# Performance work log

Measured on AMD Instinct MI355X. Metric: run time of the kernel, lower is better.

The kernel has to match this reference:

```python
import jax, jax.numpy as jnp
import numpy as np

# ---- static config (mirrors MonitorRetina init) ----
N, S, H, W = 256, 1, 144, 256        # stimulus: [N, S, H, W]
HR, WR = 144, 256                    # retina height/width
FOV_HALF_RAD = 0.5 * 75.0 * np.pi / 180.0   # Angular retina, degrees=75
GELU_GAMMA = 1.7015043497085571      # variance-preserving gain for gelu
OUT_OF_RANGE = 10.0                  # grid value for rays missing the monitor


def isotropic_grid_2d(h, w):
    """Pixel-center coordinates, isotropic (normalized by max dim), [-1,1] on the long axis."""
    m = float(max(h, w))
    y = (jnp.arange(h, dtype=jnp.float32) * 2.0 + 1.0 - h) / m
    x = (jnp.arange(w, dtype=jnp.float32) * 2.0 + 1.0 - w) / m
    gy, gx = jnp.meshgrid(y, x, indexing="ij")
    return gx, gy  # each [h, w]


def rmat_3d(ax, ay, az):
    """Batched 3D rotation matrix R = Rz @ Ry @ Rx from Euler angles, each [N]."""
    cx, sx = jnp.cos(ax), jnp.sin(ax)
    cy, sy = jnp.cos(ay), jnp.sin(ay)
    cz, sz = jnp.cos(az), jnp.sin(az)
    one, zero = jnp.ones_like(ax), jnp.zeros_like(ax)
    Rx = jnp.stack([one, zero, zero, zero, cx, -sx, zero, sx, cx], -1).reshape(-1, 3, 3)
    Ry = jnp.stack([cy, zero, sy, zero, one, zero, -sy, zero, cy], -1).reshape(-1, 3, 3)
    Rz = jnp.stack([cz, -sz, zero, sz, cz, zero, zero, zero, one], -1).reshape(-1, 3, 3)
    return jnp.einsum("nij,njk,nkl->nil", Rz, Ry, Rx)  # [N,3,3]


def retina_rays(rmat):
    """Angular retina: pixel angles -> unit ray directions, rotated per batch. [N,HR,WR,3]."""
    gx, gy = isotropic_grid_2d(HR, WR)
    ax, ay = gx * FOV_HALF_RAD, gy * FOV_HALF_RAD
    a = jnp.sqrt(ax * ax + ay * ay) + 1e-12
    sinc = jnp.sin(a) / a
    d = jnp.stack([sinc * ax, sinc * ay, jnp.cos(a)], -1)  # [HR,WR,3]
    return jnp.einsum("nij,hwj->nhwi", rmat, d)


def monitor_project(rays):
    """Plane monitor at unit distance along +z: perspective divide to isotropic grid coords. [N,HR,WR,2]."""
    rz = rays[..., 2]
    safe = rz > 1e-3
    inv = jnp.where(safe, rz, 1.0)
    gx = jnp.where(safe, rays[..., 0] / inv, OUT_OF_RANGE)
    gy = jnp.where(safe, rays[..., 1] / inv, OUT_OF_RANGE)
    return jnp.stack([gx, gy], -1)


def isotropic_grid_sample_2d(x, grid, pad_value=0.0):
    """Bilinear sample x:[N,C,H,W] at grid:[N,H',W',2] (isotropic coords), constant padding."""
    m = float(max(H, W))
    px = (grid[..., 0] * m + W - 1.0) * 0.5  # [N,H',W'] pixel coords
    py = (grid[..., 1] * m + H - 1.0) * 0.5
    x0 = jnp.floor(px)
    y0 = jnp.floor(py)
    wx = px - x0
    wy = py - y0
    x0i = x0.astype(jnp.int32)
    y0i = y0.astype(jnp.int32)

    def corner(img, yi, xi):
        valid = (xi >= 0) & (xi < W) & (yi >= 0) & (yi < H)
        v = img[:, jnp.clip(yi, 0, H - 1), jnp.clip(xi, 0, W - 1)]  # [C,H',W']
        return jnp.where(valid[None], v, pad_value)

    def one(img, y0i, x0i, wx, wy):
        v00 = corner(img, y0i, x0i)
        v01 = corner(img, y0i, x0i + 1)
        v10 = corner(img, y0i + 1, x0i)
        v11 = corner(img, y0i + 1, x0i + 1)
        return (v00 * (1 - wx) + v01 * wx) * (1 - wy) + (v10 * (1 - wx) + v11 * wx) * wy

    return jax.vmap(one)(x, y0i, x0i, wx, wy)  # [N,C,H',W']


def setup_inputs() -> dict:
    key = jax.random.key(0)
    ks = jax.random.split(key, 8)
    F, D = 16, 128
    return {
        "stimulus": jax.random.normal(ks[0], (N, S, H, W), jnp.float32),
        "perspective": jax.random.normal(ks[1], (N, F), jnp.float32),
        "W1": jax.random.normal(ks[2], (F, D), jnp.float32) / np.sqrt(F),
        "b1": jnp.zeros((D,), jnp.float32),
        "W2": jax.random.normal(ks[3], (D, D), jnp.float32) / np.sqrt(D),
        "b2": jnp.zeros((D,), jnp.float32),
        "Wp": jax.random.normal(ks[4], (D, 3), jnp.float32) * 0.05,  # proj gains init near 0
        "bp": jnp.zeros((3,), jnp.float32),
    }


def reference(stimulus, perspective, W1, b1, W2, b2, Wp, bp):
    # MLP -> 3 angles -> rotation matrix (rmat)
    h = jax.nn.gelu(perspective @ W1 + b1) * GELU_GAMMA
    h = jax.nn.gelu(h @ W2 + b2) * GELU_GAMMA
    ang = h @ Wp + bp                      # [N,3]
    rm = rmat_3d(ang[:, 0], ang[:, 1], ang[:, 2])
    rays = retina_rays(rm)                 # [N,HR,WR,3]
    grid = monitor_project(rays)           # [N,HR,WR,2]
    # monitor_pixel / retina_pixel are Raw (identity) transforms
    return isotropic_grid_sample_2d(stimulus, grid, pad_value=0.0)  # [N,S,HR,WR]
```

## Files before the change

### kernel.cpp

```cpp
#include <hip/hip_runtime.h>
#include <math.h>

#define NB    256
#define IMG_H 144
#define IMG_W 256
#define IMG_ELEMS (IMG_H * IMG_W)
#define LDS_STRIDE 260
#define HR    144
#define WR    256
#define FDIM  16
#define DDIM  128

#define FOV_HALF_RAD 0.6544984694978736f
#define GELU_GAMMA   1.7015043497085571f
#define OUT_OF_RANGE 10.0f

typedef float f32x4 __attribute__((ext_vector_type(4)));

__device__ __forceinline__ float gelu_gamma(float x) {
    const float k0 = 0.7978845608028654f;
    const float k1 = 0.044715f;
    float t = tanhf(k0 * (x + k1 * x * x * x));
    return 0.5f * x * (1.0f + t) * GELU_GAMMA;
}

__global__ void __launch_bounds__(DDIM) mlp_rmat_kernel(
    const float* __restrict__ persp,
    const float* __restrict__ W1,
    const float* __restrict__ b1,
    const float* __restrict__ W2,
    const float* __restrict__ b2,
    const float* __restrict__ Wp,
    const float* __restrict__ bp,
    float* __restrict__ Rout)
{
    const int n = blockIdx.x;
    const int d = threadIdx.x;

    __shared__ float sh1[DDIM];
    __shared__ float sh2[DDIM];
    __shared__ float ang[3];

    float acc = b1[d];
#pragma unroll
    for (int f = 0; f < FDIM; ++f)
        acc += persp[n * FDIM + f] * W1[f * DDIM + d];
    sh1[d] = gelu_gamma(acc);
    __syncthreads();

    float acc2 = b2[d];
#pragma unroll 8
    for (int k = 0; k < DDIM; ++k)
        acc2 += sh1[k] * W2[k * DDIM + d];
    sh2[d] = gelu_gamma(acc2);
    __syncthreads();

    if (d < 3) {
        float a = bp[d];
#pragma unroll 8
        for (int k = 0; k < DDIM; ++k)
            a += sh2[k] * Wp[k * 3 + d];
        ang[d] = a;
    }
    __syncthreads();

    if (d == 0) {
        float cx = cosf(ang[0]), sx = sinf(ang[0]);
        float cy = cosf(ang[1]), sy = sinf(ang[1]);
        float cz = cosf(ang[2]), sz = sinf(ang[2]);
        float* R = Rout + n * 9;
        R[0] = cz * cy;  R[1] = cz * sy * sx - sz * cx;  R[2] = cz * sy * cx + sz * sx;
        R[3] = sz * cy;  R[4] = sz * sy * sx + cz * cx;  R[5] = sz * sy * cx - cz * sx;
        R[6] = -sy;      R[7] = cy * sx;                 R[8] = cy * cx;
    }
}

__global__ void __launch_bounds__(1024, 4) retina_sample_kernel(
    const float* __restrict__ stim,
    const float* __restrict__ Rmat,
    float* __restrict__ out)
{
    __shared__ float simg[IMG_H * LDS_STRIDE];

    const int tid = threadIdx.x;
    const int n   = blockIdx.x;

    const float* Rn = Rmat + n * 9;
    const float r0 = Rn[0], r1 = Rn[1], r2 = Rn[2];
    const float r3 = Rn[3], r4 = Rn[4], r5 = Rn[5];
    const float r6 = Rn[6], r7 = Rn[7], r8 = Rn[8];

    const float* __restrict__ img = stim + (size_t)n * IMG_ELEMS;

    {
        const f32x4* __restrict__ src = (const f32x4*)img;
#pragma unroll
        for (int p = 0; p < 9; ++p) {
            const int g   = tid + p * 1024;
            const int row = g >> 6;
            const int c4  = g & 63;
            *(f32x4*)&simg[row * LDS_STRIDE + c4 * 4] = src[g];
        }
    }
    __syncthreads();

#pragma unroll
    for (int p = 0; p < 9; ++p) {
        const int g   = tid + p * 1024;
        const int px0 = g * 4;
        const int h   = px0 >> 8;
        const int w0  = px0 & 255;

        const float gy  = (2.0f * h + 1.0f - 144.0f) * (1.0f / 256.0f);
        const float ayv = gy * FOV_HALF_RAD;
        const float ay2 = ayv * ayv;

        float wx_[4], wy_[4];
        int a00[4], a01[4], a10[4], a11[4];
        bool m00[4], m01[4], m10[4], m11[4];

#pragma unroll
        for (int j = 0; j < 4; ++j) {
            const float gx  = (2.0f * (w0 + j) + 1.0f - 256.0f) * (1.0f / 256.0f);
            const float axv = gx * FOV_HALF_RAD;
            const float t   = axv * axv + ay2;

            float sc = fmaf(t, 2.7557319e-6f, -1.9841270e-4f);
            sc = fmaf(t, sc,  8.3333333e-3f);
            sc = fmaf(t, sc, -1.6666667e-1f);
            sc = fmaf(t, sc,  1.0f);

            float ca = fmaf(t, 2.4801587e-5f, -1.3888889e-3f);
            ca = fmaf(t, ca,  4.1666667e-2f);
            ca = fmaf(t, ca, -0.5f);
            ca = fmaf(t, ca,  1.0f);

            const float dx = sc * axv, dy = sc * ayv, dz = ca;

            const float rx = r0 * dx + r1 * dy + r2 * dz;
            const float ry = r3 * dx + r4 * dy + r5 * dz;
            const float rz = r6 * dx + r7 * dy + r8 * dz;

            const float inv = __builtin_amdgcn_rcpf(rz);
            const bool safe = rz > 0.001f;
            const float gxp = safe ? rx * inv : OUT_OF_RANGE;
            const float gyp = safe ? ry * inv : OUT_OF_RANGE;

            const float px = fmaf(gxp, 256.0f, (float)(IMG_W - 1)) * 0.5f;
            const float py = fmaf(gyp, 256.0f, (float)(IMG_H - 1)) * 0.5f;

            const float x0f = floorf(px), y0f = floorf(py);
            wx_[j] = px - x0f;
            wy_[j] = py - y0f;
            const int x0 = (int)x0f, y0 = (int)y0f;
            const int x1 = x0 + 1,   y1 = y0 + 1;

            const int xc0 = min(max(x0, 0), IMG_W - 1);
            const int xc1 = min(max(x1, 0), IMG_W - 1);
            const int yc0 = min(max(y0, 0), IMG_H - 1);
            const int yc1 = min(max(y1, 0), IMG_H - 1);

            m00[j] = ((unsigned)x0 < IMG_W) & ((unsigned)y0 < IMG_H);
            m01[j] = ((unsigned)x1 < IMG_W) & ((unsigned)y0 < IMG_H);
            m10[j] = ((unsigned)x0 < IMG_W) & ((unsigned)y1 < IMG_H);
            m11[j] = ((unsigned)x1 < IMG_W) & ((unsigned)y1 < IMG_H);

            a00[j] = yc0 * LDS_STRIDE + xc0;
            a01[j] = yc0 * LDS_STRIDE + xc1;
            a10[j] = yc1 * LDS_STRIDE + xc0;
            a11[j] = yc1 * LDS_STRIDE + xc1;
        }

        float v00[4], v01[4], v10[4], v11[4];
#pragma unroll
        for (int j = 0; j < 4; ++j) {
            v00[j] = simg[a00[j]];
            v01[j] = simg[a01[j]];
            v10[j] = simg[a10[j]];
            v11[j] = simg[a11[j]];
        }

        f32x4 res;
#pragma unroll
        for (int j = 0; j < 4; ++j) {
            const float c00 = m00[j] ? v00[j] : 0.0f;
            const float c01 = m01[j] ? v01[j] : 0.0f;
            const float c10 = m10[j] ? v10[j] : 0.0f;
            const float c11 = m11[j] ? v11[j] : 0.0f;
            const float top = c00 * (1.0f - wx_[j]) + c01 * wx_[j];
            const float bot = c10 * (1.0f - wx_[j]) + c11 * wx_[j];
            res[j] = top * (1.0f - wy_[j]) + bot * wy_[j];
        }

        f32x4* dst = (f32x4*)(out + (size_t)n * IMG_ELEMS + px0);
        __builtin_nontemporal_store(res, dst);
    }
}

extern "C" void kernel_launch(void* const* d_in, const int* in_sizes, int n_in,
                              void* d_out, int out_size, void* d_ws, size_t ws_size,
                              hipStream_t stream) {
    const float* stimulus    = (const float*)d_in[0];
    const float* perspective = (const float*)d_in[1];
    const float* W1          = (const float*)d_in[2];
    const float* b1          = (const float*)d_in[3];
    const float* W2          = (const float*)d_in[4];
    const float* b2          = (const float*)d_in[5];
    const float* Wp          = (const float*)d_in[6];
    const float* bp          = (const float*)d_in[7];
    float* out = (float*)d_out;

    float* Rmat = (float*)d_ws;

    mlp_rmat_kernel<<<NB, DDIM, 0, stream>>>(
        perspective, W1, b1, W2, b2, Wp, bp, Rmat);

    retina_sample_kernel<<<NB, 1024, 0, stream>>>(stimulus, Rmat, out);
}
```

Before: 118.7 us.

## Store stimulus in LDS as fp16 with zero border and split image across two blocks

```diff
diff --git a/kernel.cpp b/kernel.cpp
--- a/kernel.cpp
+++ b/kernel.cpp
@@ -5,17 +5,19 @@
 #define IMG_H 144
 #define IMG_W 256
 #define IMG_ELEMS (IMG_H * IMG_W)
-#define LDS_STRIDE 260
-#define HR    144
-#define WR    256
 #define FDIM  16
 #define DDIM  128
+
+#define LDS_STRIDE_H 264
+#define LDS_ROWS     (IMG_H + 2)
+#define SIDE_CELLS   (IMG_H * 8)
 
 #define FOV_HALF_RAD 0.6544984694978736f
 #define GELU_GAMMA   1.7015043497085571f
 #define OUT_OF_RANGE 10.0f
 
-typedef float f32x4 __attribute__((ext_vector_type(4)));
+typedef float    f32x4 __attribute__((ext_vector_type(4)));
+typedef _Float16 f16x4 __attribute__((ext_vector_type(4)));
 
 __device__ __forceinline__ float gelu_gamma(float x) {
     const float k0 = 0.7978845608028654f;
@@ -75,15 +77,16 @@
     }
 }
 
-__global__ void __launch_bounds__(1024, 4) retina_sample_kernel(
+__global__ void __launch_bounds__(1024, 8) retina_sample_kernel(
     const float* __restrict__ stim,
     const float* __restrict__ Rmat,
     float* __restrict__ out)
 {
-    __shared__ float simg[IMG_H * LDS_STRIDE];
-
-    const int tid = threadIdx.x;
-    const int n   = blockIdx.x;
+    __shared__ _Float16 simg[LDS_ROWS * LDS_STRIDE_H];
+
+    const int tid  = threadIdx.x;
+    const int n    = blockIdx.x;
+    const int half = blockIdx.y;
 
     const float* Rn = Rmat + n * 9;
     const float r0 = Rn[0], r1 = Rn[1], r2 = Rn[2];
@@ -92,6 +95,17 @@
 
     const float* __restrict__ img = stim + (size_t)n * IMG_ELEMS;
 
+    if (tid < LDS_STRIDE_H) {
+        simg[tid] = (_Float16)0.0f;
+        simg[(LDS_ROWS - 1) * LDS_STRIDE_H + tid] = (_Float16)0.0f;
+    }
+    for (int sb = tid; sb < SIDE_CELLS; sb += 1024) {
+        const int r = (sb >> 3) + 1;
+        int c = sb & 7;
+        c = (c < 4) ? c : (c + 256);
+        simg[r * LDS_STRIDE_H + c] = (_Float16)0.0f;
+    }
+
     {
         const f32x4* __restrict__ src = (const f32x4*)img;
 #pragma unroll
@@ -99,31 +113,34 @@
             const int g   = tid + p * 1024;
             const int row = g >> 6;
             const int c4  = g & 63;
-            *(f32x4*)&simg[row * LDS_STRIDE + c4 * 4] = src[g];
-        }
-    }
-    __syncthreads();
-
-#pragma unroll
-    for (int p = 0; p < 9; ++p) {
-        const int g   = tid + p * 1024;
-        const int px0 = g * 4;
+            const f16x4 hv = __builtin_convertvector(src[g], f16x4);
+            *(f16x4*)&simg[(row + 1) * LDS_STRIDE_H + 4 + c4 * 4] = hv;
+        }
+    }
+    __syncthreads();
+
+#pragma unroll
+    for (int p = 0; p < 5; ++p) {
+        const int gg = p * 1024 + tid;
+        if (gg >= 4608) break;
+        const int px0 = half * 18432 + gg * 4;
         const int h   = px0 >> 8;
         const int w0  = px0 & 255;
 
         const float gy  = (2.0f * h + 1.0f - 144.0f) * (1.0f / 256.0f);
         const float ayv = gy * FOV_HALF_RAD;
         const float ay2 = ayv * ayv;
+        const float bx = ayv * r1, by = ayv * r4, bz = ayv * r7;
 
         float wx_[4], wy_[4];
         int a00[4], a01[4], a10[4], a11[4];
-        bool m00[4], m01[4], m10[4], m11[4];
 
 #pragma unroll
         for (int j = 0; j < 4; ++j) {
-            const float gx  = (2.0f * (w0 + j) + 1.0f - 256.0f) * (1.0f / 256.0f);
-            const float axv = gx * FOV_HALF_RAD;
-            const float t   = axv * axv + ay2;
+            const float ax = fmaf((float)(w0 + j),
+                                  2.0f * FOV_HALF_RAD * (1.0f / 256.0f),
+                                  -255.0f * FOV_HALF_RAD * (1.0f / 256.0f));
+            const float t = fmaf(ax, ax, ay2);
 
             float sc = fmaf(t, 2.7557319e-6f, -1.9841270e-4f);
             sc = fmaf(t, sc,  8.3333333e-3f);
@@ -135,61 +152,49 @@
             ca = fmaf(t, ca, -0.5f);
             ca = fmaf(t, ca,  1.0f);
 
-            const float dx = sc * axv, dy = sc * ayv, dz = ca;
-
-            const float rx = r0 * dx + r1 * dy + r2 * dz;
-            const float ry = r3 * dx + r4 * dy + r5 * dz;
-            const float rz = r6 * dx + r7 * dy + r8 * dz;
+            const float rx = fmaf(ca, r2, sc * fmaf(ax, r0, bx));
+            const float ry = fmaf(ca, r5, sc * fmaf(ax, r3, by));
+            const float rz = fmaf(ca, r8, sc * fmaf(ax, r6, bz));
 
             const float inv = __builtin_amdgcn_rcpf(rz);
             const bool safe = rz > 0.001f;
             const float gxp = safe ? rx * inv : OUT_OF_RANGE;
             const float gyp = safe ? ry * inv : OUT_OF_RANGE;
 
-            const float px = fmaf(gxp, 256.0f, (float)(IMG_W - 1)) * 0.5f;
-            const float py = fmaf(gyp, 256.0f, (float)(IMG_H - 1)) * 0.5f;
+            const float px = fmaf(gxp, 128.0f, 127.5f);
+            const float py = fmaf(gyp, 128.0f, 71.5f);
 
             const float x0f = floorf(px), y0f = floorf(py);
             wx_[j] = px - x0f;
             wy_[j] = py - y0f;
             const int x0 = (int)x0f, y0 = (int)y0f;
-            const int x1 = x0 + 1,   y1 = y0 + 1;
-
-            const int xc0 = min(max(x0, 0), IMG_W - 1);
-            const int xc1 = min(max(x1, 0), IMG_W - 1);
-            const int yc0 = min(max(y0, 0), IMG_H - 1);
-            const int yc1 = min(max(y1, 0), IMG_H - 1);
-
-            m00[j] = ((unsigned)x0 < IMG_W) & ((unsigned)y0 < IMG_H);
-            m01[j] = ((unsigned)x1 < IMG_W) & ((unsigned)y0 < IMG_H);
-            m10[j] = ((unsigned)x0 < IMG_W) & ((unsigned)y1 < IMG_H);
-            m11[j] = ((unsigned)x1 < IMG_W) & ((unsigned)y1 < IMG_H);
-
-            a00[j] = yc0 * LDS_STRIDE + xc0;
-            a01[j] = yc0 * LDS_STRIDE + xc1;
-            a10[j] = yc1 * LDS_STRIDE + xc0;
-            a11[j] = yc1 * LDS_STRIDE + xc1;
+
+            const int xc0 = min(max(x0,     -1), 256);
+            const int xc1 = min(max(x0 + 1, -1), 256);
+            const int yc0 = min(max(y0,     -1), 144);
+            const int yc1 = min(max(y0 + 1, -1), 144);
+
+            const int row0 = yc0 * LDS_STRIDE_H + (LDS_STRIDE_H + 4);
+            const int row1 = yc1 * LDS_STRIDE_H + (LDS_STRIDE_H + 4);
+            a00[j] = row0 + xc0;  a01[j] = row0 + xc1;
+            a10[j] = row1 + xc0;  a11[j] = row1 + xc1;
         }
 
         float v00[4], v01[4], v10[4], v11[4];
 #pragma unroll
         for (int j = 0; j < 4; ++j) {
-            v00[j] = simg[a00[j]];
-            v01[j] = simg[a01[j]];
-            v10[j] = simg[a10[j]];
-            v11[j] = simg[a11[j]];
+            v00[j] = (float)simg[a00[j]];
+            v01[j] = (float)simg[a01[j]];
+            v10[j] = (float)simg[a10[j]];
+            v11[j] = (float)simg[a11[j]];
         }
 
         f32x4 res;
 #pragma unroll
         for (int j = 0; j < 4; ++j) {
-            const float c00 = m00[j] ? v00[j] : 0.0f;
-            const float c01 = m01[j] ? v01[j] : 0.0f;
-            const float c10 = m10[j] ? v10[j] : 0.0f;
-            const float c11 = m11[j] ? v11[j] : 0.0f;
-            const float top = c00 * (1.0f - wx_[j]) + c01 * wx_[j];
-            const float bot = c10 * (1.0f - wx_[j]) + c11 * wx_[j];
-            res[j] = top * (1.0f - wy_[j]) + bot * wy_[j];
+            const float top = fmaf(wx_[j], v01[j] - v00[j], v00[j]);
+            const float bot = fmaf(wx_[j], v11[j] - v10[j], v10[j]);
+            res[j] = fmaf(wy_[j], bot - top, top);
         }
 
         f32x4* dst = (f32x4*)(out + (size_t)n * IMG_ELEMS + px0);
@@ -215,5 +220,6 @@
     mlp_rmat_kernel<<<NB, DDIM, 0, stream>>>(
         perspective, W1, b1, W2, b2, Wp, bp, Rmat);
 
-    retina_sample_kernel<<<NB, 1024, 0, stream>>>(stimulus, Rmat, out);
-}
+    dim3 grid(NB, 2);
+    retina_sample_kernel<<<grid, 1024, 0, stream>>>(stimulus, Rmat, out);
+}
```

Result: slower. 121.2 us (+2.1%).
